# Kernel tuning notes

Hardware: AMD Instinct MI355X
Metric: run time of the kernel (lower is better)

The kernel has to match this reference:

```python
import jax, jax.numpy as jnp
import numpy as np

N = 100000          # nodes
E = 1600000         # directed edges (avg degree 16)
DIMS = [256, 256, 256, 128]


def setup_inputs() -> dict:
    key = jax.random.key(0)
    ks = jax.random.split(key, 3 + 2 * (len(DIMS) - 1))
    X = jax.random.normal(ks[0], (N, DIMS[0]), dtype=jnp.float32)
    row = jax.random.randint(ks[1], (E,), 0, N, dtype=jnp.int32)
    col = jax.random.randint(ks[2], (E,), 0, N, dtype=jnp.int32)
    inp = {"X": X, "row": row, "col": col}
    # LinearLayer params: weights ~ N(0,1)/sqrt(in_features), bias = 0
    for i in range(len(DIMS) - 1):
        d_in, d_out = DIMS[i], DIMS[i + 1]
        inp[f"W{i}"] = jax.random.normal(ks[3 + i], (d_out, d_in), dtype=jnp.float32) / jnp.sqrt(d_in)
        inp[f"b{i}"] = jnp.zeros((d_out,), dtype=jnp.float32)
    return inp


def reference(X, row, col, W0, b0, W1, b1, W2, b2):
    n = X.shape[0]
    # normalized_adjacency: A' = I + A, then D^{-1/2} A' D^{-1/2}
    loop = jnp.arange(n, dtype=row.dtype)
    rows = jnp.concatenate([row, loop])          # [E+N]
    cols = jnp.concatenate([col, loop])          # [E+N]
    vals = jnp.ones(rows.shape[0], dtype=X.dtype)
    deg = jax.ops.segment_sum(vals, rows, num_segments=n)   # row sums of A'
    norm = vals / (jnp.sqrt(deg[rows]) * jnp.sqrt(deg[cols]))  # [E+N]

    def spmm(H):  # S @ H via gather + scatter-add
        return jax.ops.segment_sum(norm[:, None] * H[cols], rows, num_segments=n)

    H = spmm(X)
    H = jax.nn.gelu(H @ W0.T + b0)
    H = spmm(H)
    H = jax.nn.gelu(H @ W1.T + b1)
    H = spmm(H)
    H = H @ W2.T + b2  # final_non_linearity = identity
    return H
```

## Files before the change

### kernel.cpp

```cpp
#include <hip/hip_runtime.h>
#include <hip/hip_bf16.h>


typedef float f32x4 __attribute__((ext_vector_type(4)));
typedef float f32x2 __attribute__((ext_vector_type(2)));
typedef _Float16 h16x8 __attribute__((ext_vector_type(8)));
typedef _Float16 h16x4 __attribute__((ext_vector_type(4)));
typedef _Float16 h16x2 __attribute__((ext_vector_type(2)));

__device__ __forceinline__ float gelu_fast(float x) {
    float u = 0.7978845608028654f * (x + 0.044715f * x * x * x);
    return x / (1.0f + __expf(-2.0f * u));
}

__global__ void count_kernel(const int* __restrict__ row, int* __restrict__ cnt,
                             int* __restrict__ rank, int e) {
    int i = blockIdx.x * blockDim.x + threadIdx.x;
    if (i < e) rank[i] = atomicAdd(&cnt[row[i]], 1);
}

__global__ void rnorm_kernel(const int* __restrict__ cnt, float* __restrict__ rnorm, int n) {
    int i = blockIdx.x * blockDim.x + threadIdx.x;
    if (i < n) rnorm[i] = rsqrtf((float)(cnt[i] + 1));
}

__global__ void scan1_kernel(const int* __restrict__ cnt, int* __restrict__ rowptr,
                             int* __restrict__ bsum, int n) {
    __shared__ int s[1024];
    int t = threadIdx.x;
    int i = blockIdx.x * 1024 + t;
    int v = (i < n) ? cnt[i] : 0;
    s[t] = v;
    __syncthreads();
    for (int off = 1; off < 1024; off <<= 1) {
        int x = (t >= off) ? s[t - off] : 0;
        __syncthreads();
        s[t] += x;
        __syncthreads();
    }
    if (i < n) rowptr[i] = s[t] - v;
    if (t == 1023) bsum[blockIdx.x] = s[1023];
}

__global__ void scan2_kernel(int* bsum, int nb) {
    __shared__ int s[128];
    int t = threadIdx.x;
    int v = (t < nb) ? bsum[t] : 0;
    s[t] = v;
    __syncthreads();
    for (int off = 1; off < 128; off <<= 1) {
        int x = (t >= off) ? s[t - off] : 0;
        __syncthreads();
        s[t] += x;
        __syncthreads();
    }
    if (t < nb) bsum[t] = s[t] - v;
}

__global__ void scan3_kernel(int* __restrict__ rowptr, const int* __restrict__ bsum, int n, int e) {
    int i = blockIdx.x * blockDim.x + threadIdx.x;
    if (i < n) rowptr[i] += bsum[i >> 10];
    if (i == 0) rowptr[n] = e;
}

__global__ void fill_kernel(const int* __restrict__ row, const int* __restrict__ col,
                            const int* __restrict__ rank,
                            const int* __restrict__ rowptr,
                            const float* __restrict__ rnorm,
                            int2* __restrict__ meta, int e) {
    int i = blockIdx.x * blockDim.x + threadIdx.x;
    if (i >= e) return;
    int r = row[i], c = col[i];
    int pos = rowptr[r] + rank[i];
    float w = rnorm[r] * rnorm[c];
    meta[pos] = make_int2(c, __float_as_int(w));
}

__global__ void splitW_kernel(const float* __restrict__ in,
                              _Float16* __restrict__ hi,
                              _Float16* __restrict__ lo, int total4) {
    int i = blockIdx.x * blockDim.x + threadIdx.x;
    if (i >= total4) return;
    f32x4 x = *(const f32x4*)(in + (size_t)i * 4);
    h16x4 h, l;
#pragma unroll
    for (int q = 0; q < 4; ++q) {
        _Float16 hb = (_Float16)x[q];
        h[q] = hb;
        l[q] = (_Float16)(x[q] - (float)hb);
    }
    *(h16x4*)(hi + (size_t)i * 4) = h;
    *(h16x4*)(lo + (size_t)i * 4) = l;
}

template <int WPL> struct HVecT;
template <> struct HVecT<4> { using T = h16x4; };
template <> struct HVecT<2> { using T = h16x2; };

template <int WPL, bool GELU, bool SPLIT>
__global__ __launch_bounds__(256) void spmm_kernel(const _Float16* __restrict__ in,
                                                   float* __restrict__ out,
                                                   _Float16* __restrict__ oat,
                                                   const int* __restrict__ rowptr,
                                                   const int2* __restrict__ meta,
                                                   const float* __restrict__ rnorm,
                                                   const float* __restrict__ bias, int n) {
    using hvec_t = typename HVecT<WPL>::T;
    constexpr int RW = 64 * WPL;
    __shared__ _Float16 h_lds[4][256];

    int t = threadIdx.x;
    int lane = t & 63;
    int w = t >> 6;
    int wid = blockIdx.x * 4 + w;
    bool active = wid < n;
    int widc = active ? wid : (n - 1);

    if (!SPLIT && !active) return;

    const _Float16* lanebase = in + lane * WPL;
    float rn = rnorm[widc];
    float sw = rn * rn;
    float acc[WPL];
    {
        hvec_t a = *(const hvec_t*)(lanebase + (size_t)widc * RW);
#pragma unroll
        for (int q = 0; q < WPL; ++q) acc[q] = sw * (float)a[q];
    }

    int e0 = rowptr[widc], e1 = rowptr[widc + 1];
    int e = e0;
    int nbatch = (e1 - e0) >> 3;
    if (nbatch > 0) {
        int2 m[8];
#pragma unroll
        for (int u = 0; u < 8; ++u) m[u] = meta[e + u];
        for (int b = 0; b < nbatch; ++b) {
            hvec_t v[8];
#pragma unroll
            for (int u = 0; u < 8; ++u) v[u] = *(const hvec_t*)(lanebase + (size_t)m[u].x * RW);
            int2 mn[8];
            bool more = (b + 1 < nbatch);
            if (more) {
#pragma unroll
                for (int u = 0; u < 8; ++u) mn[u] = meta[e + 8 + u];
            }
#pragma unroll
            for (int u = 0; u < 8; ++u) {
                float ww = __int_as_float(m[u].y);
#pragma unroll
                for (int q = 0; q < WPL; ++q) acc[q] = fmaf(ww, (float)v[u][q], acc[q]);
            }
            if (more) {
#pragma unroll
                for (int u = 0; u < 8; ++u) m[u] = mn[u];
            }
            e += 8;
        }
    }
    for (; e < e1; ++e) {
        int2 m = meta[e];
        hvec_t v = *(const hvec_t*)(lanebase + (size_t)m.x * RW);
        float ww = __int_as_float(m.y);
#pragma unroll
        for (int q = 0; q < WPL; ++q) acc[q] = fmaf(ww, (float)v[q], acc[q]);
    }

    if (SPLIT) {
        f32x4 bv = *(const f32x4*)(bias + lane * WPL);
        h16x4 h;
#pragma unroll
        for (int q = 0; q < WPL; ++q) {
            float x = acc[q] + bv[q];
            float y = GELU ? gelu_fast(x) : x;
            h[q] = (_Float16)y;
        }
        *(h16x4*)&h_lds[w][lane * 4] = h;
        __syncthreads();
        if (t < 128) {
            int kc = t >> 4;
            int g  = (t >> 2) & 3;
            int j  = t & 3;
            size_t rg = (size_t)(blockIdx.x >> 2);
            int bq = blockIdx.x & 3;
            size_t toff = ((rg * 8 + kc) * 64 + g * 16 + bq * 4 + j) * 8;
            __builtin_nontemporal_store(*(const h16x8*)&h_lds[j][kc * 32 + g * 8],
                                        (h16x8*)(oat + toff));
        }
    } else {
        f32x2 bv = *(const f32x2*)(bias + lane * WPL);
        f32x2 o;
#pragma unroll
        for (int q = 0; q < WPL; ++q) {
            float x = acc[q] + bv[q];
            o[q] = GELU ? gelu_fast(x) : x;
        }
        __builtin_nontemporal_store(o, (f32x2*)(out + (size_t)wid * RW + lane * WPL));
    }
}

template <int DO, int RT, bool XIN>
__global__ __launch_bounds__(256, 2) void dense_mfma_kernel(
        const _Float16* __restrict__ AT, const float* __restrict__ Xf,
        const _Float16* __restrict__ Whi, const _Float16* __restrict__ Wlo,
        _Float16* __restrict__ out, int n) {
    constexpr int KC = 32;
    constexpr int NCH = 256 / KC;
    constexpr int NTT = DO / 16;
    constexpr int NT = NTT / 2;
    constexpr int NFRAG = 2 * NTT;
    constexpr int BM = 2 * RT * 16;
    __shared__ h16x8 s_w[2][NFRAG * 64];

    int t = threadIdx.x;
    int lane = t & 63;
    int w = t >> 6;
    int r = lane & 15;
    int g = lane >> 4;
    int h = w & 1;
    int row0 = blockIdx.x * BM + (w >> 1) * (RT * 16);
    int n16 = (n + 15) >> 4;

    size_t argi[RT];
#pragma unroll
    for (int rt = 0; rt < RT; ++rt) {
        if (XIN) {
            int arow = row0 + rt * 16 + r;
            if (arow >= n) arow = n - 1;
            argi[rt] = (size_t)arow;
        } else {
            int rg = (row0 >> 4) + rt;
            if (rg >= n16) rg = n16 - 1;
            argi[rt] = (size_t)rg;
        }
    }

    f32x4 acc[RT][NT];
#pragma unroll
    for (int rt = 0; rt < RT; ++rt)
#pragma unroll
        for (int nt = 0; nt < NT; ++nt) acc[rt][nt] = (f32x4){0.f, 0.f, 0.f, 0.f};

    auto stage = [&](int c, int b) {
#pragma unroll
        for (int i = 0; i < NFRAG / 4; ++i) {
            int s = t + i * 256;
            int sl = s & 63;
            int f = s >> 6;
            int ntf = f % NTT;
            int op = f / NTT;
            const _Float16* src = op ? Wlo : Whi;
            const _Float16* gsrc =
                &src[(size_t)(ntf * 16 + (sl & 15)) * 256 + c * KC + ((sl >> 4) << 3)];
            __builtin_amdgcn_global_load_lds(
                (const __attribute__((address_space(1))) void*)gsrc,
                (__attribute__((address_space(3))) void*)&s_w[b][s], 16, 0, 0);
        }
    };

    h16x8 aC[2][RT];
    f32x4 nf[RT][2];

    auto prefetchA = [&](int c, int set) {
#pragma unroll
        for (int rt = 0; rt < RT; ++rt) {
            if (XIN) {
                const float* src = &Xf[argi[rt] * 256 + c * KC + g * 8];
                nf[rt][0] = *(const f32x4*)src;
                nf[rt][1] = *(const f32x4*)(src + 4);
            } else {
                aC[set][rt] = *(const h16x8*)&AT[((argi[rt] * 8 + c) * 64 + lane) * 8];
            }
        }
    };
    auto commitA = [&](int set) {
        if (XIN) {
#pragma unroll
            for (int rt = 0; rt < RT; ++rt) {
                h16x8 hh;
#pragma unroll
                for (int q = 0; q < 4; ++q) {
                    hh[q] = (_Float16)nf[rt][0][q];
                    hh[q + 4] = (_Float16)nf[rt][1][q];
                }
                aC[set][rt] = hh;
            }
        }
    };

    stage(0, 0);
    prefetchA(0, 0);
    asm volatile("s_waitcnt vmcnt(0)" ::: "memory");
    __builtin_amdgcn_sched_barrier(0);
    commitA(0);
    __builtin_amdgcn_s_barrier();
    __builtin_amdgcn_sched_barrier(0);

#pragma unroll
    for (int c = 0; c < NCH; ++c) {
        const int b = c & 1;
        if (c + 1 < NCH) {
            stage(c + 1, b ^ 1);
            prefetchA(c + 1, b ^ 1);
            constexpr int VM = (NFRAG / 4) + (XIN ? 2 * RT : RT);
            asm volatile("s_waitcnt vmcnt(%0)" :: "i"(VM) : "memory");
        } else {
            asm volatile("s_waitcnt vmcnt(0)" ::: "memory");
        }
        __builtin_amdgcn_sched_barrier(0);
        __builtin_amdgcn_s_barrier();
        __builtin_amdgcn_sched_barrier(0);

#pragma unroll
        for (int nt = 0; nt < NT; ++nt) {
            int ntf = h * NT + nt;
            h16x8 wh = s_w[b][ntf * 64 + lane];
            h16x8 wl = s_w[b][(NTT + ntf) * 64 + lane];
#pragma unroll
            for (int rt = 0; rt < RT; ++rt) {
                acc[rt][nt] = __builtin_amdgcn_mfma_f32_16x16x32_f16(aC[b][rt], wh, acc[rt][nt], 0, 0, 0);
                acc[rt][nt] = __builtin_amdgcn_mfma_f32_16x16x32_f16(aC[b][rt], wl, acc[rt][nt], 0, 0, 0);
            }
        }
        __builtin_amdgcn_sched_barrier(0);
        if (c + 1 < NCH) commitA(b ^ 1);
        __builtin_amdgcn_s_barrier();
    }

#pragma unroll
    for (int rt = 0; rt < RT; ++rt) {
#pragma unroll
        for (int nt = 0; nt < NT; ++nt) {
            int ccol = (h * NT + nt) * 16 + r;
#pragma unroll
            for (int j = 0; j < 4; ++j) {
                int rr = row0 + rt * 16 + g * 4 + j;
                if (rr < n) out[(size_t)rr * DO + ccol] = (_Float16)acc[rt][nt][j];
            }
        }
    }
}

extern "C" void kernel_launch(void* const* d_in, const int* in_sizes, int n_in,
                              void* d_out, int out_size, void* d_ws, size_t ws_size,
                              hipStream_t stream) {
    const float* X  = (const float*)d_in[0];
    const int* row  = (const int*)d_in[1];
    const int* col  = (const int*)d_in[2];
    const float* W0 = (const float*)d_in[3];
    const float* b0 = (const float*)d_in[4];
    const float* W1 = (const float*)d_in[5];
    const float* b1 = (const float*)d_in[6];
    const float* W2 = (const float*)d_in[7];
    const float* b2 = (const float*)d_in[8];

    int n = in_sizes[0] / 256;
    int e = in_sizes[1];
    size_t n16pad = (size_t)((n + 15) / 16) * 16;

    char* ws = (char*)d_ws;
    size_t off = 0;
    auto alloc = [&](size_t bytes) {
        void* p = ws + off;
        off += (bytes + 255) & ~(size_t)255;
        return p;
    };
    _Float16* AT  = (_Float16*)alloc(n16pad * 256 * 2);
    _Float16* Dh  = (_Float16*)alloc((size_t)n * 256 * 2);
    _Float16* W0h = (_Float16*)alloc(256 * 256 * 2);
    _Float16* W0l = (_Float16*)alloc(256 * 256 * 2);
    _Float16* W1h = (_Float16*)alloc(256 * 256 * 2);
    _Float16* W1l = (_Float16*)alloc(256 * 256 * 2);
    _Float16* W2h = (_Float16*)alloc(256 * 128 * 2);
    _Float16* W2l = (_Float16*)alloc(256 * 128 * 2);
    int*   cnt    = (int*)alloc((size_t)n * 4);
    int*   rank   = (int*)alloc((size_t)e * 4);
    float* rnorm  = (float*)alloc((size_t)n * 4);
    int*   rowptr = (int*)alloc(((size_t)n + 1) * 4);
    int*   bsum   = (int*)alloc(512);
    int2*  meta   = (int2*)alloc((size_t)e * 8);

    (void)hipMemsetAsync(cnt, 0, (size_t)n * 4, stream);

    int gE = (e + 255) / 256;
    int gN = (n + 255) / 256;
    int nb = (n + 1023) / 1024;

    count_kernel<<<gE, 256, 0, stream>>>(row, cnt, rank, e);
    rnorm_kernel<<<gN, 256, 0, stream>>>(cnt, rnorm, n);
    scan1_kernel<<<nb, 1024, 0, stream>>>(cnt, rowptr, bsum, n);
    scan2_kernel<<<1, 128, 0, stream>>>(bsum, nb);
    scan3_kernel<<<gN, 256, 0, stream>>>(rowptr, bsum, n, e);
    fill_kernel<<<gE, 256, 0, stream>>>(row, col, rank, rowptr, rnorm, meta, e);

    splitW_kernel<<<(16384 + 255) / 256, 256, 0, stream>>>(W0, W0h, W0l, 16384);
    splitW_kernel<<<(16384 + 255) / 256, 256, 0, stream>>>(W1, W1h, W1l, 16384);
    splitW_kernel<<<(8192 + 255) / 256, 256, 0, stream>>>(W2, W2h, W2l, 8192);

    int gS  = (n + 3) / 4;
    int gMd = (n + 127) / 128;

    dense_mfma_kernel<256, 4, true><<<gMd, 256, 0, stream>>>(nullptr, X, W0h, W0l, Dh, n);
    spmm_kernel<4, true, true><<<gS, 256, 0, stream>>>(Dh, nullptr, AT, rowptr, meta, rnorm, b0, n);
    dense_mfma_kernel<256, 4, false><<<gMd, 256, 0, stream>>>(AT, nullptr, W1h, W1l, Dh, n);
    spmm_kernel<4, true, true><<<gS, 256, 0, stream>>>(Dh, nullptr, AT, rowptr, meta, rnorm, b1, n);
    dense_mfma_kernel<128, 4, false><<<gMd, 256, 0, stream>>>(AT, nullptr, W2h, W2l, Dh, n);
    spmm_kernel<2, false, false><<<gS, 256, 0, stream>>>(Dh, (float*)d_out, nullptr, rowptr, meta, rnorm, b2, n);
}
```

Measured before the change: 658.6 us.

## Process two rows per wavefront in SpMM with wider per-lane gathers

```diff
diff --git a/kernel.cpp b/kernel.cpp
--- a/kernel.cpp
+++ b/kernel.cpp
@@ -93,11 +93,11 @@
     *(h16x4*)(lo + (size_t)i * 4) = l;
 }
 
-template <int WPL> struct HVecT;
-template <> struct HVecT<4> { using T = h16x4; };
-template <> struct HVecT<2> { using T = h16x2; };
-
-template <int WPL, bool GELU, bool SPLIT>
+template <int CL> struct CVecT;
+template <> struct CVecT<8> { using T = h16x8; };
+template <> struct CVecT<4> { using T = h16x4; };
+
+template <int D, bool GELU, bool SPLIT>
 __global__ __launch_bounds__(256) void spmm_kernel(const _Float16* __restrict__ in,
                                                    float* __restrict__ out,
                                                    _Float16* __restrict__ oat,
@@ -105,97 +105,90 @@
                                                    const int2* __restrict__ meta,
                                                    const float* __restrict__ rnorm,
                                                    const float* __restrict__ bias, int n) {
-    using hvec_t = typename HVecT<WPL>::T;
-    constexpr int RW = 64 * WPL;
-    __shared__ _Float16 h_lds[4][256];
+    constexpr int CL = D / 32;
+    using cvec_t = typename CVecT<CL>::T;
+    __shared__ _Float16 h_lds[8][256];
 
     int t = threadIdx.x;
     int lane = t & 63;
     int w = t >> 6;
-    int wid = blockIdx.x * 4 + w;
-    bool active = wid < n;
-    int widc = active ? wid : (n - 1);
-
-    if (!SPLIT && !active) return;
-
-    const _Float16* lanebase = in + lane * WPL;
-    float rn = rnorm[widc];
+    int sub = lane & 31;
+    int rowsel = lane >> 5;
+    int wid = blockIdx.x * 8 + w * 2 + rowsel;
+    if (wid >= n) wid = n - 1;
+
+    const _Float16* lanebase = in + sub * CL;
+    float rn = rnorm[wid];
     float sw = rn * rn;
-    float acc[WPL];
+    float acc[CL];
     {
-        hvec_t a = *(const hvec_t*)(lanebase + (size_t)widc * RW);
-#pragma unroll
-        for (int q = 0; q < WPL; ++q) acc[q] = sw * (float)a[q];
-    }
-
-    int e0 = rowptr[widc], e1 = rowptr[widc + 1];
-    int e = e0;
-    int nbatch = (e1 - e0) >> 3;
-    if (nbatch > 0) {
-        int2 m[8];
-#pragma unroll
-        for (int u = 0; u < 8; ++u) m[u] = meta[e + u];
-        for (int b = 0; b < nbatch; ++b) {
-            hvec_t v[8];
-#pragma unroll
-            for (int u = 0; u < 8; ++u) v[u] = *(const hvec_t*)(lanebase + (size_t)m[u].x * RW);
-            int2 mn[8];
-            bool more = (b + 1 < nbatch);
-            if (more) {
-#pragma unroll
-                for (int u = 0; u < 8; ++u) mn[u] = meta[e + 8 + u];
-            }
-#pragma unroll
-            for (int u = 0; u < 8; ++u) {
-                float ww = __int_as_float(m[u].y);
-#pragma unroll
-                for (int q = 0; q < WPL; ++q) acc[q] = fmaf(ww, (float)v[u][q], acc[q]);
-            }
-            if (more) {
-#pragma unroll
-                for (int u = 0; u < 8; ++u) m[u] = mn[u];
-            }
-            e += 8;
-        }
-    }
-    for (; e < e1; ++e) {
-        int2 m = meta[e];
-        hvec_t v = *(const hvec_t*)(lanebase + (size_t)m.x * RW);
-        float ww = __int_as_float(m.y);
-#pragma unroll
-        for (int q = 0; q < WPL; ++q) acc[q] = fmaf(ww, (float)v[q], acc[q]);
+        cvec_t a = *(const cvec_t*)(lanebase + (size_t)wid * D);
+#pragma unroll
+        for (int q = 0; q < CL; ++q) acc[q] = sw * (float)a[q];
+    }
+
+    int e0 = rowptr[wid], e1 = rowptr[wid + 1];
+    int ne = e1 - e0;
+    int maxb = (ne + 3) >> 2;
+    int elast = (e1 > e0) ? (e1 - 1) : 0;
+
+    int2 m[4];
+    auto loadM = [&](int b) {
+#pragma unroll
+        for (int u = 0; u < 4; ++u) {
+            int idx = e0 + b * 4 + u;
+            int eu = idx < e1 ? idx : elast;
+            int2 mm = meta[eu];
+            if (idx >= e1) mm.y = 0;
+            m[u] = mm;
+        }
+    };
+    if (maxb > 0) loadM(0);
+    for (int b = 0; b < maxb; ++b) {
+        cvec_t v[4];
+#pragma unroll
+        for (int u = 0; u < 4; ++u)
+            v[u] = *(const cvec_t*)(lanebase + (size_t)m[u].x * D);
+        float wts[4];
+#pragma unroll
+        for (int u = 0; u < 4; ++u) wts[u] = __int_as_float(m[u].y);
+        if (b + 1 < maxb) loadM(b + 1);
+#pragma unroll
+        for (int u = 0; u < 4; ++u)
+#pragma unroll
+            for (int q = 0; q < CL; ++q) acc[q] = fmaf(wts[u], (float)v[u][q], acc[q]);
     }
 
     if (SPLIT) {
-        f32x4 bv = *(const f32x4*)(bias + lane * WPL);
-        h16x4 h;
-#pragma unroll
-        for (int q = 0; q < WPL; ++q) {
-            float x = acc[q] + bv[q];
-            float y = GELU ? gelu_fast(x) : x;
-            h[q] = (_Float16)y;
-        }
-        *(h16x4*)&h_lds[w][lane * 4] = h;
+        f32x4 bv0 = *(const f32x4*)(bias + sub * CL);
+        f32x4 bv1 = *(const f32x4*)(bias + sub * CL + 4);
+        h16x8 h;
+#pragma unroll
+        for (int q = 0; q < 4; ++q) {
+            float x0 = acc[q] + bv0[q];
+            float x1 = acc[q + 4] + bv1[q];
+            h[q] = (_Float16)(GELU ? gelu_fast(x0) : x0);
+            h[q + 4] = (_Float16)(GELU ? gelu_fast(x1) : x1);
+        }
+        *(h16x8*)&h_lds[w * 2 + rowsel][sub * 8] = h;
         __syncthreads();
-        if (t < 128) {
-            int kc = t >> 4;
-            int g  = (t >> 2) & 3;
-            int j  = t & 3;
-            size_t rg = (size_t)(blockIdx.x >> 2);
-            int bq = blockIdx.x & 3;
-            size_t toff = ((rg * 8 + kc) * 64 + g * 16 + bq * 4 + j) * 8;
-            __builtin_nontemporal_store(*(const h16x8*)&h_lds[j][kc * 32 + g * 8],
-                                        (h16x8*)(oat + toff));
-        }
+        int kc = t >> 5;
+        int g  = (t >> 3) & 3;
+        int j  = t & 7;
+        size_t rg = (size_t)(blockIdx.x >> 1);
+        int half = blockIdx.x & 1;
+        size_t toff = ((rg * 8 + kc) * 64 + g * 16 + half * 8 + j) * 8;
+        __builtin_nontemporal_store(*(const h16x8*)&h_lds[j][kc * 32 + g * 8],
+                                    (h16x8*)(oat + toff));
     } else {
-        f32x2 bv = *(const f32x2*)(bias + lane * WPL);
-        f32x2 o;
-#pragma unroll
-        for (int q = 0; q < WPL; ++q) {
+        f32x4 bv = *(const f32x4*)(bias + sub * CL);
+        f32x4 o;
+#pragma unroll
+        for (int q = 0; q < CL; ++q) {
             float x = acc[q] + bv[q];
             o[q] = GELU ? gelu_fast(x) : x;
         }
-        __builtin_nontemporal_store(o, (f32x2*)(out + (size_t)wid * RW + lane * WPL));
+        __builtin_nontemporal_store(o, (f32x4*)(out + (size_t)wid * D + sub * CL));
     }
 }
 
@@ -397,13 +390,13 @@
     splitW_kernel<<<(16384 + 255) / 256, 256, 0, stream>>>(W1, W1h, W1l, 16384);
     splitW_kernel<<<(8192 + 255) / 256, 256, 0, stream>>>(W2, W2h, W2l, 8192);
 
-    int gS  = (n + 3) / 4;
+    int gS  = (n + 7) / 8;
     int gMd = (n + 127) / 128;
 
     dense_mfma_kernel<256, 4, true><<<gMd, 256, 0, stream>>>(nullptr, X, W0h, W0l, Dh, n);
-    spmm_kernel<4, true, true><<<gS, 256, 0, stream>>>(Dh, nullptr, AT, rowptr, meta, rnorm, b0, n);
+    spmm_kernel<256, true, true><<<gS, 256, 0, stream>>>(Dh, nullptr, AT, rowptr, meta, rnorm, b0, n);
     dense_mfma_kernel<256, 4, false><<<gMd, 256, 0, stream>>>(AT, nullptr, W1h, W1l, Dh, n);
-    spmm_kernel<4, true, true><<<gS, 256, 0, stream>>>(Dh, nullptr, AT, rowptr, meta, rnorm, b1, n);
+    spmm_kernel<256, true, true><<<gS, 256, 0, stream>>>(Dh, nullptr, AT, rowptr, meta, rnorm, b1, n);
     dense_mfma_kernel<128, 4, false><<<gMd, 256, 0, stream>>>(AT, nullptr, W2h, W2l, Dh, n);
-    spmm_kernel<2, false, false><<<gS, 256, 0, stream>>>(Dh, (float*)d_out, nullptr, rowptr, meta, rnorm, b2, n);
-}
+    spmm_kernel<128, false, false><<<gS, 256, 0, stream>>>(Dh, (float*)d_out, nullptr, rowptr, meta, rnorm, b2, n);
+}
```

After: 581.8 us. -11.7%, faster.
